# Kernel optimization log

Measured on AMD Instinct MI355X. Metric: run time of the kernel, lower is better.

## Reference

```python
import jax, jax.numpy as jnp
import numpy as np

NEG_SLOPE = 0.2  # PyG GATConv default negative_slope


def gat_conv(x, src, dst, W, a_src, a_dst, b, concat):
    """One PyG-style GATConv (eval mode, self-loops already added to src/dst).
    x: [N, Fin], W: [Fin, H*C], a_src/a_dst: [H, C], b: [H*C] or [C].
    """
    N = x.shape[0]
    H, C = a_src.shape
    h = (x @ W).reshape(N, H, C)                       # [N,H,C]
    alpha_s = jnp.sum(h * a_src, axis=-1)              # [N,H]
    alpha_d = jnp.sum(h * a_dst, axis=-1)              # [N,H]
    e = alpha_s[src] + alpha_d[dst]                    # [E,H]
    e = jax.nn.leaky_relu(e, NEG_SLOPE)
    # scatter-softmax over incoming edges of each destination node
    m = jax.ops.segment_max(e, dst, num_segments=N)    # [N,H]
    p = jnp.exp(e - m[dst])                            # [E,H]
    s = jax.ops.segment_sum(p, dst, num_segments=N)    # [N,H]
    alpha = p / s[dst]                                 # [E,H]
    msg = h[src] * alpha[:, :, None]                   # [E,H,C]
    out = jax.ops.segment_sum(msg, dst, num_segments=N)  # [N,H,C]
    out = out.reshape(N, H * C) if concat else out.mean(axis=1)
    return out + b


def setup_inputs() -> dict:
    key = jax.random.key(0)
    ks = jax.random.split(key, 12)
    N, E = 50000, 800000
    IN_C, HID, HEADS, OUT_C = 1, 32, 4, 1
    HW = HID * HEADS  # 128
    x = jax.random.normal(ks[0], (N, IN_C), dtype=jnp.float32)
    edge_index = jax.random.randint(ks[1], (2, E), 0, N, dtype=jnp.int64)
    g = 0.1
    inp = {
        "x": x,
        "edge_index": edge_index,
        "W1": jax.random.normal(ks[2], (IN_C, HW), dtype=jnp.float32) * g,
        "a_src1": jax.random.normal(ks[3], (HEADS, HID), dtype=jnp.float32) * g,
        "a_dst1": jax.random.normal(ks[4], (HEADS, HID), dtype=jnp.float32) * g,
        "b1": jnp.zeros((HW,), dtype=jnp.float32),
        "W2": jax.random.normal(ks[5], (HW, HW), dtype=jnp.float32) * g,
        "a_src2": jax.random.normal(ks[6], (HEADS, HID), dtype=jnp.float32) * g,
        "a_dst2": jax.random.normal(ks[7], (HEADS, HID), dtype=jnp.float32) * g,
        "b2": jnp.zeros((HW,), dtype=jnp.float32),
        "W3": jax.random.normal(ks[8], (HW, OUT_C), dtype=jnp.float32) * g,
        "a_src3": jax.random.normal(ks[9], (1, OUT_C), dtype=jnp.float32) * g,
        "a_dst3": jax.random.normal(ks[10], (1, OUT_C), dtype=jnp.float32) * g,
        "b3": jnp.zeros((OUT_C,), dtype=jnp.float32),
    }
    return inp


def reference(x, edge_index, W1, a_src1, a_dst1, b1, W2, a_src2, a_dst2, b2,
              W3, a_src3, a_dst3, b3):
    N = x.shape[0]
    loop = jnp.arange(N, dtype=edge_index.dtype)
    # PyG GATConv add_self_loops=True (each layer): add once, reused by all layers
    src = jnp.concatenate([edge_index[0], loop])
    dst = jnp.concatenate([edge_index[1], loop])
    h = gat_conv(x, src, dst, W1, a_src1, a_dst1, b1, concat=True)
    h = jax.nn.elu(h)  # dropout is identity in eval mode
    h = gat_conv(h, src, dst, W2, a_src2, a_dst2, b2, concat=True)
    h = jax.nn.elu(h)
    out = gat_conv(h, src, dst, W3, a_src3, a_dst3, b3, concat=False)
    return out
```

## Files before the change

### kernel.cpp

```cpp
#include <hip/hip_runtime.h>
#include <math.h>

#define NEG_SLOPE 0.2f
#define MAXDEG 64

typedef _Float16 hv4 __attribute__((ext_vector_type(4)));
typedef _Float16 hv8 __attribute__((ext_vector_type(8)));
typedef unsigned short usv4 __attribute__((ext_vector_type(4)));

static __device__ __forceinline__ float leaky(float v){ return v > 0.f ? v : NEG_SLOPE * v; }
static __device__ __forceinline__ float eluf(float v){ return v > 0.f ? v : expm1f(v); }
static __device__ __forceinline__ float eluf_fast(float v){ return v > 0.f ? v : __expf(v) - 1.f; }

__global__ void __launch_bounds__(256) scatter_k(const int* __restrict__ esrc, const int* __restrict__ edst,
                                                 int* __restrict__ cnt, unsigned short* __restrict__ csr,
                                                 int Eg, int Etot, int N){
  const int slot = blockIdx.x & 7;
  const int lo = (int)(((long long)slot * N) >> 3);
  const int hi = (int)(((long long)(slot + 1) * N) >> 3);
  const int stride = (gridDim.x >> 3) * blockDim.x;
  for (int e = (blockIdx.x >> 3) * blockDim.x + threadIdx.x; e < Etot; e += stride){
    int s, d;
    if (e < Eg){ d = edst[e]; if (d < lo || d >= hi) continue; s = esrc[e]; }
    else { s = d = e - Eg; if (d < lo || d >= hi) continue; }
    int pos = atomicAdd(&cnt[d], 1);
    if (pos < MAXDEG) csr[((size_t)d << 6) + pos] = (unsigned short)s;
  }
}

__global__ void dots1_k(const float* __restrict__ W1, const float* __restrict__ a_s,
                        const float* __restrict__ a_d, float* __restrict__ dAdD){
  int t = threadIdx.x;
  float ps = W1[t] * a_s[t];
  float pd = W1[t] * a_d[t];
  #pragma unroll
  for (int off = 16; off; off >>= 1){
    ps += __shfl_xor(ps, off, 32);
    pd += __shfl_xor(pd, off, 32);
  }
  if ((t & 31) == 0){ dAdD[t >> 5] = ps; dAdD[4 + (t >> 5)] = pd; }
}

__global__ void __launch_bounds__(256) r1_k(const int* __restrict__ cnt, const unsigned short* __restrict__ csr,
                                            const float* __restrict__ x, const float* __restrict__ dAdD,
                                            float4* __restrict__ r4, int N){
  int node = blockIdx.x * 32 + (threadIdx.x >> 3);
  if (node >= N) return;
  const int q = threadIdx.x & 7;
  const int start = node << 6;
  int dg = cnt[node]; dg = dg < MAXDEG ? dg : MAXDEG;
  const int end = start + dg;
  const float xd = x[node];
  float dA0 = dAdD[0], dA1 = dAdD[1], dA2 = dAdD[2], dA3 = dAdD[3];
  float e0d = xd * dAdD[4], e1d = xd * dAdD[5], e2d = xd * dAdD[6], e3d = xd * dAdD[7];

  float s0 = 0.f, s1 = 0.f, s2 = 0.f, s3 = 0.f;
  float t0 = 0.f, t1 = 0.f, t2 = 0.f, t3 = 0.f;
  int i = start + q;
  if (i < end){
    int idx = csr[i];
    while (true){
      const int inext = i + 8;
      const bool more = inext < end;
      const int idxn = csr[more ? inext : i];
      float xs = x[idx];
      float p0 = __expf(leaky(xs * dA0 + e0d));
      float p1 = __expf(leaky(xs * dA1 + e1d));
      float p2 = __expf(leaky(xs * dA2 + e2d));
      float p3 = __expf(leaky(xs * dA3 + e3d));
      s0 += p0; s1 += p1; s2 += p2; s3 += p3;
      t0 += p0 * xs; t1 += p1 * xs; t2 += p2 * xs; t3 += p3 * xs;
      if (!more) break;
      idx = idxn; i = inext;
    }
  }
  #pragma unroll
  for (int off = 4; off; off >>= 1){
    s0 += __shfl_xor(s0, off, 8); t0 += __shfl_xor(t0, off, 8);
    s1 += __shfl_xor(s1, off, 8); t1 += __shfl_xor(t1, off, 8);
    s2 += __shfl_xor(s2, off, 8); t2 += __shfl_xor(t2, off, 8);
    s3 += __shfl_xor(s3, off, 8); t3 += __shfl_xor(t3, off, 8);
  }
  if (q == 0) r4[node] = make_float4(t0 / s0, t1 / s1, t2 / s2, t3 / s3);
}

__global__ void __launch_bounds__(256) gemm2_k(const float4* __restrict__ r4,
                                               const float* __restrict__ W1f, const float* __restrict__ b1f,
                                               const float* __restrict__ W,
                                               const float* __restrict__ a_s, const float* __restrict__ a_d,
                                               _Float16* __restrict__ hh, float* __restrict__ as_, float* __restrict__ ad_,
                                               int N){
  __shared__ float sA[128][68];
  __shared__ _Float16 sW[2][16][128];
  const int t = threadIdx.x;
  const int n0 = blockIdx.x * 64;
  const int tx = t & 15, ty = t >> 4;
  const int c0 = tx * 8, r0 = ty * 4;

  const int wk = t >> 5;
  const int wq = t & 31;

  float4 rw0, rw1;
  auto gloadW = [&](int k0){
    rw0 = *(const float4*)&W[(size_t)(k0 + wk) * 128 + wq * 4];
    rw1 = *(const float4*)&W[(size_t)(k0 + wk + 8) * 128 + wq * 4];
  };
  auto sstoreW = [&](int buf){
    hv4 a = {(_Float16)rw0.x, (_Float16)rw0.y, (_Float16)rw0.z, (_Float16)rw0.w};
    hv4 b = {(_Float16)rw1.x, (_Float16)rw1.y, (_Float16)rw1.z, (_Float16)rw1.w};
    *(hv4*)&sW[buf][wk][wq * 4]     = a;
    *(hv4*)&sW[buf][wk + 8][wq * 4] = b;
  };

  {
    const int nl = t & 63, q = t >> 6;
    const int gn = n0 + nl;
    float r = 0.f;
    const bool valid = (gn < N);
    if (valid){
      float4 rv = r4[gn];
      r = (q == 0) ? rv.x : (q == 1) ? rv.y : (q == 2) ? rv.z : rv.w;
    }
    #pragma unroll
    for (int j = 0; j < 32; ++j){
      const int c = q * 32 + j;
      float v = W1f[c] * r + b1f[c];
      v = eluf_fast(v);
      sA[c][nl] = valid ? v : 0.f;
    }
  }

  float acc[4][8];
  #pragma unroll
  for (int r = 0; r < 4; ++r)
    #pragma unroll
    for (int c = 0; c < 8; ++c) acc[r][c] = 0.f;

  gloadW(0); sstoreW(0); __syncthreads();

  #pragma unroll 1
  for (int tile = 0; tile < 8; ++tile){
    const int buf = tile & 1;
    if (tile < 7) gloadW((tile + 1) * 16);
    #pragma unroll
    for (int k = 0; k < 16; ++k){
      float4 aa = *(const float4*)&sA[tile * 16 + k][r0];
      hv8 wh = *(const hv8*)&sW[buf][k][c0];
      float av[4] = {aa.x, aa.y, aa.z, aa.w};
      float wv[8];
      #pragma unroll
      for (int c = 0; c < 8; ++c) wv[c] = (float)wh[c];
      #pragma unroll
      for (int r = 0; r < 4; ++r)
        #pragma unroll
        for (int c = 0; c < 8; ++c) acc[r][c] += av[r] * wv[c];
    }
    if (tile < 7){ sstoreW(1 - buf); __syncthreads(); }
  }

  float asv[8], adv[8];
  #pragma unroll
  for (int c = 0; c < 8; ++c){ asv[c] = a_s[c0 + c]; adv[c] = a_d[c0 + c]; }

  const int hd  = tx >> 2;
  const int off = (tx & 3) * 8;

  #pragma unroll
  for (int r = 0; r < 4; ++r){
    int n = n0 + r0 + r;
    if (n >= N) continue;
    hv8 hv;
    #pragma unroll
    for (int c = 0; c < 8; ++c) hv[c] = (_Float16)acc[r][c];
    *(hv8*)&hh[((size_t)hd * N + n) * 32 + off] = hv;
    float ps = 0.f, pd = 0.f;
    #pragma unroll
    for (int c = 0; c < 8; ++c){ ps += acc[r][c] * asv[c]; pd += acc[r][c] * adv[c]; }
    ps += __shfl_xor(ps, 1); ps += __shfl_xor(ps, 2);
    pd += __shfl_xor(pd, 1); pd += __shfl_xor(pd, 2);
    if ((tx & 3) == 0){
      as_[(size_t)hd * N + n] = ps;
      ad_[(size_t)hd * N + n] = pd;
    }
  }
}

__global__ void __launch_bounds__(256) node_aggr2_k(const int* __restrict__ cnt, const unsigned short* __restrict__ csr,
                                                    const float* __restrict__ as_, const float* __restrict__ ad_,
                                                    const _Float16* __restrict__ hh, const float* __restrict__ b2,
                                                    const float* __restrict__ W3, float* __restrict__ h3, int N){
  const int slot   = blockIdx.x & 7;
  const int chunk  = blockIdx.x >> 3;
  const int head   = slot >> 1;
  const int parity = slot & 1;
  const int t  = threadIdx.x;
  const int nl = t >> 2;
  const int q  = t & 3;
  const int base = chunk * 256 + parity * 128 + nl;
  const float* __restrict__ ash = as_ + (size_t)head * N;
  const _Float16* __restrict__ hhh = hh + (size_t)head * N * 32 + q * 8;
  const int c0 = head * 32 + q * 8;

  #pragma unroll 1
  for (int half = 0; half < 2; ++half){
    const int node = base + half * 64;
    if (node >= N) continue;
    const int start = node << 6;
    int dg = cnt[node]; dg = dg < MAXDEG ? dg : MAXDEG;
    const int end = start + dg;
    const float adv = ad_[(size_t)head * N + node];

    float s = 0.f;
    float acc[8] = {0.f, 0.f, 0.f, 0.f, 0.f, 0.f, 0.f, 0.f};
    int i = start;

    const int iend4 = start + (dg & ~3);
    if (i < iend4){
      usv4 ia = *(const usv4*)&csr[i];
      while (i < iend4){
        const int inext = i + 4;
        const int ipf = (inext < iend4) ? inext : i;
        usv4 ib = *(const usv4*)&csr[ipf];
        const int sx = ia.x, sy = ia.y, sz = ia.z, sw = ia.w;
        const int mysrc = (q == 0) ? sx : (q == 1) ? sy : (q == 2) ? sz : sw;
        float aq = ash[mysrc];
        hv8 h0 = *(const hv8*)&hhh[(size_t)sx * 32];
        hv8 h1 = *(const hv8*)&hhh[(size_t)sy * 32];
        hv8 h2 = *(const hv8*)&hhh[(size_t)sz * 32];
        hv8 h3v = *(const hv8*)&hhh[(size_t)sw * 32];
        float pq = __expf(leaky(aq + adv));
        float p0 = __shfl(pq, 0, 4);
        float p1 = __shfl(pq, 1, 4);
        float p2 = __shfl(pq, 2, 4);
        float p3 = __shfl(pq, 3, 4);
        s += (p0 + p1) + (p2 + p3);
        #pragma unroll
        for (int c = 0; c < 8; ++c)
          acc[c] += (float)h0[c]*p0 + (float)h1[c]*p1 + (float)h2[c]*p2 + (float)h3v[c]*p3;
        ia = ib; i = inext;
      }
    }
    for (; i < end; ++i){
      int src = csr[i];
      float p = __expf(leaky(ash[src] + adv));
      hv8 hv = *(const hv8*)&hhh[(size_t)src * 32];
      s += p;
      #pragma unroll
      for (int c = 0; c < 8; ++c) acc[c] += (float)hv[c] * p;
    }

    const float inv = 1.f / s;
    float part = 0.f;
    #pragma unroll
    for (int c = 0; c < 8; ++c){
      float v = eluf_fast(acc[c] * inv + b2[c0 + c]);
      part += v * W3[c0 + c];
    }
    part += __shfl_xor(part, 1, 4);
    part += __shfl_xor(part, 2, 4);
    if (q == 0) unsafeAtomicAdd(&h3[node], part);
  }
}

__global__ void __launch_bounds__(256) node_aggr3_k(const int* __restrict__ cnt, const unsigned short* __restrict__ csr,
                                                    const float* __restrict__ h3,
                                                    const float* __restrict__ a_s3, const float* __restrict__ a_d3,
                                                    const float* __restrict__ b3,
                                                    float* __restrict__ out, int N){
  int node = blockIdx.x * 32 + (threadIdx.x >> 3);
  if (node >= N) return;
  int q = threadIdx.x & 7;
  const int start = node << 6;
  int dg = cnt[node]; dg = dg < MAXDEG ? dg : MAXDEG;
  const int end = start + dg;
  const float a_s3v = a_s3[0];
  const float adv = a_d3[0] * h3[node];
  float s = 0.f, acc = 0.f;
  int i = start + q;
  if (i < end){
    int idx = csr[i];
    while (true){
      const int inext = i + 8;
      const bool more = inext < end;
      const int idxn = csr[more ? inext : i];
      float hv = h3[idx];
      float p = __expf(leaky(a_s3v * hv + adv));
      s += p; acc += hv * p;
      if (!more) break;
      idx = idxn; i = inext;
    }
  }
  #pragma unroll
  for (int off = 4; off; off >>= 1){
    s += __shfl_xor(s, off, 8);
    acc += __shfl_xor(acc, off, 8);
  }
  if (q == 0) out[node] = acc / s + b3[0];
}

extern "C" void kernel_launch(void* const* d_in, const int* in_sizes, int n_in,
                              void* d_out, int out_size, void* d_ws, size_t ws_size,
                              hipStream_t stream){
  const float* x   = (const float*)d_in[0];
  const int*   ei  = (const int*)  d_in[1];
  const float* W1  = (const float*)d_in[2];
  const float* as1 = (const float*)d_in[3];
  const float* ad1 = (const float*)d_in[4];
  const float* b1  = (const float*)d_in[5];
  const float* W2  = (const float*)d_in[6];
  const float* as2 = (const float*)d_in[7];
  const float* ad2 = (const float*)d_in[8];
  const float* b2  = (const float*)d_in[9];
  const float* W3  = (const float*)d_in[10];
  const float* as3 = (const float*)d_in[11];
  const float* ad3 = (const float*)d_in[12];
  const float* b3  = (const float*)d_in[13];

  const int N    = in_sizes[0];
  const int Eg   = in_sizes[1] / 2;
  const int Etot = Eg + N;
  const int* esrc = ei;
  const int* edst = ei + Eg;

  char* w = (char*)d_ws;
  auto carve = [&](size_t bytes)->char*{
    char* p = w; w += (bytes + 15) & ~size_t(15); return p;
  };
  _Float16* hbuf = (_Float16*)carve((size_t)N * 128 * 2);
  float* r4b    = (float*)carve((size_t)N * 4 * 4);
  float* asb    = (float*)carve((size_t)N * 4 * 4);
  float* adb    = (float*)carve((size_t)N * 4 * 4);
  float* h3b    = (float*)carve((size_t)N * 4);
  int*   cnt    = (int*)  carve((size_t)N * 4);
  unsigned short* csr16 = (unsigned short*)carve((size_t)N * MAXDEG * 2);
  float* dAdD   = (float*)carve(8 * 4);

  const int B = 256;
  auto cdiv = [](int a, int b){ return (a + b - 1) / b; };

  hipMemsetAsync(cnt, 0, (size_t)N * 4, stream);
  hipMemsetAsync(h3b, 0, (size_t)N * 4, stream);
  scatter_k<<<128 * 8, B, 0, stream>>>(esrc, edst, cnt, csr16, Eg, Etot, N);

  dots1_k<<<1, 128, 0, stream>>>(W1, as1, ad1, dAdD);
  r1_k<<<cdiv(N, 32), B, 0, stream>>>(cnt, csr16, x, dAdD, (float4*)r4b, N);

  gemm2_k<<<cdiv(N, 64), B, 0, stream>>>((const float4*)r4b, W1, b1,
                                         W2, as2, ad2, hbuf, asb, adb, N);
  node_aggr2_k<<<cdiv(N, 256) * 8, B, 0, stream>>>(cnt, csr16, asb, adb,
                                                   hbuf, b2, W3, h3b, N);

  node_aggr3_k<<<cdiv(N, 32), B, 0, stream>>>(cnt, csr16, h3b, as3, ad3, b3, (float*)d_out, N);
}
```

Baseline: 231.6 us.

## Fuse layer-1 attention aggregation and head dot products into the GEMM kernel

```diff
diff --git a/kernel.cpp b/kernel.cpp
--- a/kernel.cpp
+++ b/kernel.cpp
@@ -28,63 +28,9 @@
   }
 }
 
-__global__ void dots1_k(const float* __restrict__ W1, const float* __restrict__ a_s,
-                        const float* __restrict__ a_d, float* __restrict__ dAdD){
-  int t = threadIdx.x;
-  float ps = W1[t] * a_s[t];
-  float pd = W1[t] * a_d[t];
-  #pragma unroll
-  for (int off = 16; off; off >>= 1){
-    ps += __shfl_xor(ps, off, 32);
-    pd += __shfl_xor(pd, off, 32);
-  }
-  if ((t & 31) == 0){ dAdD[t >> 5] = ps; dAdD[4 + (t >> 5)] = pd; }
-}
-
-__global__ void __launch_bounds__(256) r1_k(const int* __restrict__ cnt, const unsigned short* __restrict__ csr,
-                                            const float* __restrict__ x, const float* __restrict__ dAdD,
-                                            float4* __restrict__ r4, int N){
-  int node = blockIdx.x * 32 + (threadIdx.x >> 3);
-  if (node >= N) return;
-  const int q = threadIdx.x & 7;
-  const int start = node << 6;
-  int dg = cnt[node]; dg = dg < MAXDEG ? dg : MAXDEG;
-  const int end = start + dg;
-  const float xd = x[node];
-  float dA0 = dAdD[0], dA1 = dAdD[1], dA2 = dAdD[2], dA3 = dAdD[3];
-  float e0d = xd * dAdD[4], e1d = xd * dAdD[5], e2d = xd * dAdD[6], e3d = xd * dAdD[7];
-
-  float s0 = 0.f, s1 = 0.f, s2 = 0.f, s3 = 0.f;
-  float t0 = 0.f, t1 = 0.f, t2 = 0.f, t3 = 0.f;
-  int i = start + q;
-  if (i < end){
-    int idx = csr[i];
-    while (true){
-      const int inext = i + 8;
-      const bool more = inext < end;
-      const int idxn = csr[more ? inext : i];
-      float xs = x[idx];
-      float p0 = __expf(leaky(xs * dA0 + e0d));
-      float p1 = __expf(leaky(xs * dA1 + e1d));
-      float p2 = __expf(leaky(xs * dA2 + e2d));
-      float p3 = __expf(leaky(xs * dA3 + e3d));
-      s0 += p0; s1 += p1; s2 += p2; s3 += p3;
-      t0 += p0 * xs; t1 += p1 * xs; t2 += p2 * xs; t3 += p3 * xs;
-      if (!more) break;
-      idx = idxn; i = inext;
-    }
-  }
-  #pragma unroll
-  for (int off = 4; off; off >>= 1){
-    s0 += __shfl_xor(s0, off, 8); t0 += __shfl_xor(t0, off, 8);
-    s1 += __shfl_xor(s1, off, 8); t1 += __shfl_xor(t1, off, 8);
-    s2 += __shfl_xor(s2, off, 8); t2 += __shfl_xor(t2, off, 8);
-    s3 += __shfl_xor(s3, off, 8); t3 += __shfl_xor(t3, off, 8);
-  }
-  if (q == 0) r4[node] = make_float4(t0 / s0, t1 / s1, t2 / s2, t3 / s3);
-}
-
-__global__ void __launch_bounds__(256) gemm2_k(const float4* __restrict__ r4,
+__global__ void __launch_bounds__(256) gemm2_k(const int* __restrict__ cnt, const unsigned short* __restrict__ csr,
+                                               const float* __restrict__ x,
+                                               const float* __restrict__ as1, const float* __restrict__ ad1,
                                                const float* __restrict__ W1f, const float* __restrict__ b1f,
                                                const float* __restrict__ W,
                                                const float* __restrict__ a_s, const float* __restrict__ a_d,
@@ -92,10 +38,56 @@
                                                int N){
   __shared__ float sA[128][68];
   __shared__ _Float16 sW[2][16][128];
+  __shared__ float sR[64][4];
+  __shared__ float sDot[8];
   const int t = threadIdx.x;
   const int n0 = blockIdx.x * 64;
   const int tx = t & 15, ty = t >> 4;
   const int c0 = tx * 8, r0 = ty * 4;
+
+  if (t < 128){
+    float ps = W1f[t] * as1[t];
+    float pd = W1f[t] * ad1[t];
+    #pragma unroll
+    for (int off = 16; off; off >>= 1){
+      ps += __shfl_xor(ps, off, 32);
+      pd += __shfl_xor(pd, off, 32);
+    }
+    if ((t & 31) == 0){ sDot[t >> 5] = ps; sDot[4 + (t >> 5)] = pd; }
+  }
+  __syncthreads();
+
+  {
+    const int nl2 = t >> 2, q = t & 3;
+    const int gn = n0 + nl2;
+    if (gn < N){
+      const float xd = x[gn];
+      const float dA = sDot[q];
+      const float ed = xd * sDot[4 + q];
+      const int start = gn << 6;
+      int dg = cnt[gn]; dg = dg < MAXDEG ? dg : MAXDEG;
+      const int endi = start + dg;
+      float s = 0.f, tt = 0.f;
+      float rres = 0.f;
+      if (dg > 0){
+        int i = start;
+        int idx = csr[i];
+        while (true){
+          const int inext = i + 1;
+          const bool more = inext < endi;
+          const int idxn = csr[more ? inext : i];
+          float xs = x[idx];
+          float p = __expf(leaky(xs * dA + ed));
+          s += p; tt += p * xs;
+          if (!more) break;
+          idx = idxn; i = inext;
+        }
+        rres = tt / s;
+      }
+      sR[nl2][q] = rres;
+    }
+  }
+  __syncthreads();
 
   const int wk = t >> 5;
   const int wq = t & 31;
@@ -115,12 +107,8 @@
   {
     const int nl = t & 63, q = t >> 6;
     const int gn = n0 + nl;
-    float r = 0.f;
     const bool valid = (gn < N);
-    if (valid){
-      float4 rv = r4[gn];
-      r = (q == 0) ? rv.x : (q == 1) ? rv.y : (q == 2) ? rv.z : rv.w;
-    }
+    float r = valid ? sR[nl][q] : 0.f;
     #pragma unroll
     for (int j = 0; j < 32; ++j){
       const int c = q * 32 + j;
@@ -327,13 +315,11 @@
     char* p = w; w += (bytes + 15) & ~size_t(15); return p;
   };
   _Float16* hbuf = (_Float16*)carve((size_t)N * 128 * 2);
-  float* r4b    = (float*)carve((size_t)N * 4 * 4);
   float* asb    = (float*)carve((size_t)N * 4 * 4);
   float* adb    = (float*)carve((size_t)N * 4 * 4);
   float* h3b    = (float*)carve((size_t)N * 4);
   int*   cnt    = (int*)  carve((size_t)N * 4);
   unsigned short* csr16 = (unsigned short*)carve((size_t)N * MAXDEG * 2);
-  float* dAdD   = (float*)carve(8 * 4);
 
   const int B = 256;
   auto cdiv = [](int a, int b){ return (a + b - 1) / b; };
@@ -342,10 +328,7 @@
   hipMemsetAsync(h3b, 0, (size_t)N * 4, stream);
   scatter_k<<<128 * 8, B, 0, stream>>>(esrc, edst, cnt, csr16, Eg, Etot, N);
 
-  dots1_k<<<1, 128, 0, stream>>>(W1, as1, ad1, dAdD);
-  r1_k<<<cdiv(N, 32), B, 0, stream>>>(cnt, csr16, x, dAdD, (float4*)r4b, N);
-
-  gemm2_k<<<cdiv(N, 64), B, 0, stream>>>((const float4*)r4b, W1, b1,
+  gemm2_k<<<cdiv(N, 64), B, 0, stream>>>(cnt, csr16, x, as1, ad1, W1, b1,
                                          W2, as2, ad2, hbuf, asb, adb, N);
   node_aggr2_k<<<cdiv(N, 256) * 8, B, 0, stream>>>(cnt, csr16, asb, adb,
                                                    hbuf, b2, W3, h3b, N);
```

Result: slower. 236.6 us (+2.1%).
